# Kernel tuning notes

Measured on AMD Instinct MI355X. Metric: run time of the kernel, lower is better.

## Reference

```python
import jax, jax.numpy as jnp
import numpy as np

B, C, N = 4, 64, 64      # batch, channels (=2*hidden), set size
E = 128                  # set_emb
H = 32                   # hidden_channels


def _unif(k, shape, fan_in):
    lim = 1.0 / np.sqrt(fan_in)
    return jax.random.uniform(k, shape, jnp.float32, -lim, lim)


def setup_inputs() -> dict:
    key = jax.random.key(0)
    ks = jax.random.split(key, 17)
    inp = {"x": jax.random.normal(ks[0], (B, C, N, N), jnp.float32)}
    # set_convs: Linear(4,E) -> ReLU -> Linear(E,E) -> ReLU -> Linear(E,E) -> ReLU -> Linear(E,2)
    inp["W1"] = _unif(ks[1], (4, E), 4);   inp["b1"] = _unif(ks[2], (E,), 4)
    inp["W2"] = _unif(ks[3], (E, E), E);   inp["b2"] = _unif(ks[4], (E,), E)
    inp["W3"] = _unif(ks[5], (E, E), E);   inp["b3"] = _unif(ks[6], (E,), E)
    inp["W4"] = _unif(ks[7], (E, 2), E);   inp["b4"] = _unif(ks[8], (2,), E)
    # channel_fc: 1x1 convs C->128->256->256->H with ReLU between
    inp["Wc1"] = _unif(ks[9], (C, 128), C);     inp["bc1"] = _unif(ks[10], (128,), C)
    inp["Wc2"] = _unif(ks[11], (128, 256), 128); inp["bc2"] = _unif(ks[12], (256,), 128)
    inp["Wc3"] = _unif(ks[13], (256, 256), 256); inp["bc3"] = _unif(ks[14], (256,), 256)
    inp["Wc4"] = _unif(ks[15], (256, H), 256);   inp["bc4"] = _unif(ks[16], (H,), 256)
    return inp


def reference(x, W1, b1, W2, b2, W3, b3, W4, b4,
              Wc1, bc1, Wc2, bc2, Wc3, bc3, Wc4, bc4):
    Bx, Cx, n, _ = x.shape
    # ---- g_x_2to2: gather per-pair 2x2 blocks ----
    d = jnp.diagonal(x, axis1=-2, axis2=-1)              # (B,C,n)
    i = jnp.arange(1, n)[:, None]                        # (n-1,1)
    k = jnp.broadcast_to(jnp.arange(n)[None, :], (n - 1, n))
    j = (k + i) % n                                      # (n-1,n)
    d1 = jnp.broadcast_to(d[:, :, None, :], (Bx, Cx, n - 1, n))  # x[k,k]
    d2 = x[:, :, k, j]                                   # x[k,(k+i)%n]
    d3 = x[:, :, j, k]                                   # x[(k+i)%n,k]
    d4 = d[:, :, j]                                      # x[(k+i)%n,(k+i)%n]
    h = jnp.stack([d1, d2, d3, d4], -1).reshape(Bx, Cx, n * (n - 1), 4)
    # ---- set_convs MLP ----
    h = jax.nn.relu(h @ W1 + b1)
    h = jax.nn.relu(h @ W2 + b2)
    h = jax.nn.relu(h @ W3 + b3)
    h = h @ W4 + b4                                      # (B,C,n(n-1),2)
    # ---- sum_ginv_x_2to2 scatter + coeff ----
    rows = k.reshape(-1)
    cols = j.reshape(-1)
    out = jnp.zeros((Bx, Cx, n, n), x.dtype).at[:, :, rows, cols].set(h[..., 1])
    diag_vals = h[..., 0].reshape(Bx, Cx, n - 1, n).sum(2) / (n - 1)  # coeff diag 1/(n-1)
    out = out + diag_vals[..., :, None] * jnp.eye(n, dtype=x.dtype)
    # ---- channel_fc: 1x1 convs ----
    y = jax.nn.relu(jnp.einsum('bcnm,cd->bdnm', out, Wc1) + bc1[:, None, None])
    y = jax.nn.relu(jnp.einsum('bcnm,cd->bdnm', y, Wc2) + bc2[:, None, None])
    y = jax.nn.relu(jnp.einsum('bcnm,cd->bdnm', y, Wc3) + bc3[:, None, None])
    y = jnp.einsum('bcnm,cd->bdnm', y, Wc4) + bc4[:, None, None]
    return y
```

## Files before the change

kernel.cpp:

```cpp
#include <hip/hip_runtime.h>

typedef __attribute__((ext_vector_type(4))) float f32x4;
typedef __attribute__((ext_vector_type(8))) short s16x8;
typedef __attribute__((ext_vector_type(4))) short s16x4;

__device__ __forceinline__ short f2bf(float f) {
    unsigned u = __builtin_bit_cast(unsigned, f);
    u += 0x7fffu + ((u >> 16) & 1u);
    return (short)(u >> 16);
}
__device__ __forceinline__ short f2bf_fast(float f) {
    unsigned u = __builtin_bit_cast(unsigned, f);
    return (short)((u + 0x8000u) >> 16);
}

__global__ void k_prep(const float* __restrict__ W2, const float* __restrict__ W3,
                       const float* __restrict__ W4,
                       const float* __restrict__ Wc1, const float* __restrict__ Wc2,
                       const float* __restrict__ Wc3, const float* __restrict__ Wc4,
                       short* __restrict__ W2T, short* __restrict__ W3T,
                       float* __restrict__ W4T,
                       short* __restrict__ Wc1T, short* __restrict__ Wc2T,
                       short* __restrict__ Wc3T, short* __restrict__ Wc4T)
{
    int tid = blockIdx.x * 256 + threadIdx.x;
    if (tid < 16384) {
        int n = tid >> 7, k = tid & 127;
        W2T[tid] = f2bf(W2[k * 128 + n]);
        W3T[tid] = f2bf(W3[k * 128 + n]);
    }
    if (tid < 256) {
        int s = tid >> 7, k = tid & 127;
        W4T[tid] = W4[k * 2 + s];
    }
    if (tid < 8192) {
        int n = tid >> 6, c = tid & 63;
        Wc1T[tid] = f2bf(Wc1[c * 128 + n]);
    }
    if (tid < 32768) {
        int n = tid >> 7, k = tid & 127;
        Wc2T[tid] = f2bf(Wc2[k * 256 + n]);
    }
    if (tid < 65536) {
        int n = tid >> 8, k = tid & 255;
        Wc3T[tid] = f2bf(Wc3[k * 256 + n]);
    }
    if (tid < 8192) {
        int n = tid >> 8, k = tid & 255;
        Wc4T[tid] = f2bf(Wc4[k * 32 + n]);
    }
}

__global__ __launch_bounds__(256, 4)
void k_phase1(const float* __restrict__ x,
              const float* __restrict__ W1, const float* __restrict__ b1,
              const short* __restrict__ W2T, const float* __restrict__ b2,
              const short* __restrict__ W3T, const float* __restrict__ b3,
              const float* __restrict__ W4T, const float* __restrict__ b4,
              short* __restrict__ outb, float* __restrict__ diagpart)
{
    __shared__ short hA[64 * 128];
    __shared__ short hB[64 * 128];
    __shared__ float red[4][4][16][2];
    const int t = threadIdx.x;
    const int lane = t & 63;
    const int w = t >> 6;
    const int lr = lane & 15;
    const int hi = lane >> 4;
    const int b = blockIdx.x;
    const int bc = b / 63;
    const int r  = b - bc * 63;

    {
        const int kk = t & 63;
        const int e0 = __builtin_amdgcn_readfirstlane((t >> 6) * 32);
        const int jj = (kk + r + 1) & 63;
        const float* xb = x + bc * 4096;
        float f0 = xb[kk * 65], f1 = xb[kk * 64 + jj];
        float f2 = xb[jj * 64 + kk], f3 = xb[jj * 65];
#pragma unroll
        for (int eo = 0; eo < 32; eo += 8) {
            s16x8 pk;
#pragma unroll
            for (int q = 0; q < 8; ++q) {
                int e = e0 + eo + q;
                float a = fmaf(f3, W1[384 + e], fmaf(f2, W1[256 + e],
                          fmaf(f1, W1[128 + e], fmaf(f0, W1[e], b1[e]))));
                pk[q] = f2bf_fast(fmaxf(a, 0.f));
            }
            int off = (kk * 256 + (e0 + eo) * 2) ^ ((kk & 7) << 4);
            *(s16x8*)((char*)hA + off) = pk;
        }
    }
    __syncthreads();

    const int n0 = w * 32;

    f32x4 acc[4][2] = {};
#pragma unroll
    for (int ks = 0; ks < 4; ++ks) {
        const int kb = ks * 32 + hi * 8;
        s16x8 aw[2], bh[4];
#pragma unroll
        for (int nf = 0; nf < 2; ++nf)
            aw[nf] = *(const s16x8*)(W2T + (n0 + nf * 16 + lr) * 128 + kb);
#pragma unroll
        for (int mf = 0; mf < 4; ++mf) {
            int off = ((mf * 16 + lr) * 256 + kb * 2) ^ ((lr & 7) << 4);
            bh[mf] = *(const s16x8*)((const char*)hA + off);
        }
#pragma unroll
        for (int mf = 0; mf < 4; ++mf)
#pragma unroll
            for (int nf = 0; nf < 2; ++nf)
                acc[mf][nf] = __builtin_amdgcn_mfma_f32_16x16x32_bf16(aw[nf], bh[mf], acc[mf][nf], 0, 0, 0);
    }
    {
        f32x4 bv[2];
#pragma unroll
        for (int nf = 0; nf < 2; ++nf)
            bv[nf] = *(const f32x4*)(b2 + n0 + nf * 16 + 4 * hi);
#pragma unroll
        for (int mf = 0; mf < 4; ++mf) {
            int m = mf * 16 + lr;
#pragma unroll
            for (int nf = 0; nf < 2; ++nf) {
                s16x4 pk;
#pragma unroll
                for (int q = 0; q < 4; ++q)
                    pk[q] = f2bf_fast(fmaxf(acc[mf][nf][q] + bv[nf][q], 0.f));
                int off = (m * 256 + (n0 + nf * 16 + 4 * hi) * 2) ^ ((m & 7) << 4);
                *(s16x4*)((char*)hB + off) = pk;
            }
        }
    }
    __syncthreads();

    f32x4 acc3[4][2] = {};
#pragma unroll
    for (int ks = 0; ks < 4; ++ks) {
        const int kb = ks * 32 + hi * 8;
        s16x8 aw[2], bh[4];
#pragma unroll
        for (int nf = 0; nf < 2; ++nf)
            aw[nf] = *(const s16x8*)(W3T + (n0 + nf * 16 + lr) * 128 + kb);
#pragma unroll
        for (int mf = 0; mf < 4; ++mf) {
            int off = ((mf * 16 + lr) * 256 + kb * 2) ^ ((lr & 7) << 4);
            bh[mf] = *(const s16x8*)((const char*)hB + off);
        }
#pragma unroll
        for (int mf = 0; mf < 4; ++mf)
#pragma unroll
            for (int nf = 0; nf < 2; ++nf)
                acc3[mf][nf] = __builtin_amdgcn_mfma_f32_16x16x32_bf16(aw[nf], bh[mf], acc3[mf][nf], 0, 0, 0);
    }
    {
        f32x4 bv[2], w40[2], w41[2];
#pragma unroll
        for (int nf = 0; nf < 2; ++nf) {
            bv[nf]  = *(const f32x4*)(b3 + n0 + nf * 16 + 4 * hi);
            w40[nf] = *(const f32x4*)(W4T + n0 + nf * 16 + 4 * hi);
            w41[nf] = *(const f32x4*)(W4T + 128 + n0 + nf * 16 + 4 * hi);
        }
#pragma unroll
        for (int mf = 0; mf < 4; ++mf) {
            float s0 = 0.f, s1 = 0.f;
#pragma unroll
            for (int nf = 0; nf < 2; ++nf)
#pragma unroll
                for (int q = 0; q < 4; ++q) {
                    float h = fmaxf(acc3[mf][nf][q] + bv[nf][q], 0.f);
                    s0 = fmaf(h, w40[nf][q], s0);
                    s1 = fmaf(h, w41[nf][q], s1);
                }
            s0 += __shfl_xor(s0, 16, 64); s0 += __shfl_xor(s0, 32, 64);
            s1 += __shfl_xor(s1, 16, 64); s1 += __shfl_xor(s1, 32, 64);
            if (hi == 0) { red[w][mf][lr][0] = s0; red[w][mf][lr][1] = s1; }
        }
    }
    __syncthreads();
    if (t < 128) {
        int k = t & 63, s = t >> 6;
        int mf = k >> 4, lr2 = k & 15;
        float v = red[0][mf][lr2][s] + red[1][mf][lr2][s]
                + red[2][mf][lr2][s] + red[3][mf][lr2][s] + b4[s];
        if (s) {
            int jj = (k + r + 1) & 63;
            outb[bc * 4096 + k * 64 + jj] = f2bf(v);
        } else {
            diagpart[b * 64 + k] = v;
        }
    }
}

__global__ void k_diag(const float* __restrict__ diagpart, short* __restrict__ outb)
{
    __shared__ float rds[256];
    const int t = threadIdx.x, bcq = blockIdx.x;
    const int kx = t & 63, q = t >> 6;
    const float* p = diagpart + bcq * 4032 + kx;
    int r0 = q * 16, r1 = (r0 + 16 < 63) ? r0 + 16 : 63;
    float s = 0.f;
    for (int rr = r0; rr < r1; ++rr) s += p[rr * 64];
    rds[t] = s;
    __syncthreads();
    if (t < 64) {
        float v = (rds[t] + rds[t + 64] + rds[t + 128] + rds[t + 192]) * (1.0f / 63.0f);
        outb[bcq * 4096 + t * 65] = f2bf(v);
    }
}

template<int K, int NT, int NWN, int N_OUT, bool RELU, int SRC, int DST>
__global__ __launch_bounds__(256, 4)
void k_chan(const void* __restrict__ srcv, const short* __restrict__ WT,
            const float* __restrict__ bias, void* __restrict__ dstv)
{
    constexpr int MF = (NWN == 4) ? 2 : 1;
    constexpr int NF = NT / (16 * NWN);
    constexpr int KS = K / 32;
    __shared__ short A[32 * K];
    const int t = threadIdx.x, lane = t & 63, w = t >> 6;
    const int lr = lane & 15, hi = lane >> 4;
    const int m0 = blockIdx.x * 32;
    const int col0 = blockIdx.y * NT;
    const int wn = w & (NWN - 1);
    const int wm = w >> ((NWN == 4) ? 2 : 1);
    const int n0 = col0 + wn * 16 * NF;

    if (SRC == 0) {
        const short* src = (const short*)srcv;
#pragma unroll
        for (int i = t * 8; i < 32 * K; i += 2048) {
            int row = i / K, kk2 = i - row * K;
            s16x8 v = *(const s16x8*)(src + (size_t)m0 * K + i);
            int off = (row * (K * 2) + kk2 * 2) ^ ((row & 7) << 4);
            *(s16x8*)((char*)A + off) = v;
        }
    } else {
        const short* src = (const short*)srcv;
        int bb = blockIdx.x >> 7;
        int nm0 = (blockIdx.x & 127) * 32;
        int c = t & 63, rq = t >> 6;
        s16x8 v = *(const s16x8*)(src + ((size_t)(bb * 64 + c)) * 4096 + nm0 + rq * 8);
#pragma unroll
        for (int q = 0; q < 8; ++q) {
            int row = rq * 8 + q;
            int off = (row * (K * 2) + c * 2) ^ ((row & 7) << 4);
            *(short*)((char*)A + off) = v[q];
        }
    }
    __syncthreads();

    f32x4 acc[MF][NF] = {};
#pragma unroll
    for (int ks = 0; ks < KS; ++ks) {
        const int kb = ks * 32 + hi * 8;
        s16x8 aw[NF], bh[MF];
#pragma unroll
        for (int nf = 0; nf < NF; ++nf)
            aw[nf] = *(const s16x8*)(WT + (size_t)(n0 + nf * 16 + lr) * K + kb);
#pragma unroll
        for (int mf = 0; mf < MF; ++mf) {
            int row = (wm * MF + mf) * 16 + lr;
            int off = (row * (K * 2) + kb * 2) ^ ((lr & 7) << 4);
            bh[mf] = *(const s16x8*)((const char*)A + off);
        }
#pragma unroll
        for (int mf = 0; mf < MF; ++mf)
#pragma unroll
            for (int nf = 0; nf < NF; ++nf)
                acc[mf][nf] = __builtin_amdgcn_mfma_f32_16x16x32_bf16(aw[nf], bh[mf], acc[mf][nf], 0, 0, 0);
    }

    f32x4 bv[NF];
#pragma unroll
    for (int nf = 0; nf < NF; ++nf)
        bv[nf] = *(const f32x4*)(bias + n0 + nf * 16 + 4 * hi);
#pragma unroll
    for (int mf = 0; mf < MF; ++mf) {
        int mrow = (wm * MF + mf) * 16 + lr;
#pragma unroll
        for (int nf = 0; nf < NF; ++nf) {
            if (DST == 0) {
                s16x4 pk;
#pragma unroll
                for (int q = 0; q < 4; ++q) {
                    float v2 = acc[mf][nf][q] + bv[nf][q];
                    if (RELU) v2 = fmaxf(v2, 0.f);
                    pk[q] = f2bf_fast(v2);
                }
                *(s16x4*)((short*)dstv + (size_t)(m0 + mrow) * N_OUT + n0 + nf * 16 + 4 * hi) = pk;
            } else {
                int bb = blockIdx.x >> 7;
                int nm = (blockIdx.x & 127) * 32 + mrow;
#pragma unroll
                for (int q = 0; q < 4; ++q) {
                    int n = n0 + nf * 16 + 4 * hi + q;
                    ((float*)dstv)[(size_t)(bb * 32 + n) * 4096 + nm] = acc[mf][nf][q] + bv[nf][q];
                }
            }
        }
    }
}

extern "C" void kernel_launch(void* const* d_in, const int* in_sizes, int n_in,
                              void* d_out, int out_size, void* d_ws, size_t ws_size,
                              hipStream_t stream)
{
    const float* x   = (const float*)d_in[0];
    const float* W1  = (const float*)d_in[1];
    const float* b1  = (const float*)d_in[2];
    const float* W2  = (const float*)d_in[3];
    const float* b2  = (const float*)d_in[4];
    const float* W3  = (const float*)d_in[5];
    const float* b3  = (const float*)d_in[6];
    const float* W4  = (const float*)d_in[7];
    const float* b4  = (const float*)d_in[8];
    const float* Wc1 = (const float*)d_in[9];
    const float* bc1 = (const float*)d_in[10];
    const float* Wc2 = (const float*)d_in[11];
    const float* bc2 = (const float*)d_in[12];
    const float* Wc3 = (const float*)d_in[13];
    const float* bc3 = (const float*)d_in[14];
    const float* Wc4 = (const float*)d_in[15];
    const float* bc4 = (const float*)d_in[16];
    float* out = (float*)d_out;

    char* ws = (char*)d_ws;
    short* y3       = (short*)(ws);
    short* outb     = (short*)(ws + (8u  << 20));
    float* diagpart = (float*)(ws + (10u << 20));
    short* y2       = (short*)(ws + (8u  << 20));
    short* y1       = (short*)(ws + (16u << 20));

    size_t off = 20u << 20;
    short* W2T  = (short*)(ws + off); off += 16384 * 2;
    short* W3T  = (short*)(ws + off); off += 16384 * 2;
    short* Wc1T = (short*)(ws + off); off += 8192 * 2;
    short* Wc2T = (short*)(ws + off); off += 32768 * 2;
    short* Wc3T = (short*)(ws + off); off += 65536 * 2;
    short* Wc4T = (short*)(ws + off); off += 8192 * 2;
    float* W4T  = (float*)(ws + off); off += 256 * 4;

    k_prep<<<256, 256, 0, stream>>>(W2, W3, W4, Wc1, Wc2, Wc3, Wc4,
                                    W2T, W3T, W4T, Wc1T, Wc2T, Wc3T, Wc4T);
    k_phase1<<<16128, 256, 0, stream>>>(x, W1, b1, W2T, b2, W3T, b3, W4T, b4,
                                        outb, diagpart);
    k_diag<<<256, 256, 0, stream>>>(diagpart, outb);
    k_chan< 64, 128, 4, 128, true,  1, 0><<<dim3(512, 1), 256, 0, stream>>>(outb, Wc1T, bc1, y1);
    k_chan<128, 128, 4, 256, true,  0, 0><<<dim3(512, 2), 256, 0, stream>>>(y1, Wc2T, bc2, y2);
    k_chan<256, 128, 4, 256, true,  0, 0><<<dim3(512, 2), 256, 0, stream>>>(y2, Wc3T, bc3, y3);
    k_chan<256,  32, 2,  32, false, 0, 1><<<dim3(512, 1), 256, 0, stream>>>(y3, Wc4T, bc4, out);
}
```

Measured before the change: 278.9 us.

## Fuse four channel 1x1-conv layers into one kernel and preload MLP weights

Replaces the four separate channel_fc kernels with a single kernel that keeps each 32-row tile's intermediate activations in two shared-memory ping-pong buffers, so the y1/y2/y3 bf16 intermediates never go to global memory. This also cuts three kernel launches. Separately, phase1 now loads all W2/W3 weight fragments into registers up front, before the first GEMM, instead of inside the k-loops. The cost is more register pressure in phase1, which may lower occupancy. The fused kernel has 512 blocks, each computing all output columns, so there is less parallelism per layer.

New measurement: 253.6 us. -9.1%, faster.

```diff
diff --git a/kernel.cpp b/kernel.cpp
--- a/kernel.cpp
+++ b/kernel.cpp
@@ -71,6 +71,17 @@
     const int bc = b / 63;
     const int r  = b - bc * 63;
 
+    const int n0 = w * 32;
+
+    s16x8 aw2[4][2], aw3[4][2];
+#pragma unroll
+    for (int ks = 0; ks < 4; ++ks)
+#pragma unroll
+        for (int nf = 0; nf < 2; ++nf) {
+            aw2[ks][nf] = *(const s16x8*)(W2T + (n0 + nf * 16 + lr) * 128 + ks * 32 + hi * 8);
+            aw3[ks][nf] = *(const s16x8*)(W3T + (n0 + nf * 16 + lr) * 128 + ks * 32 + hi * 8);
+        }
+
     {
         const int kk = t & 63;
         const int e0 = __builtin_amdgcn_readfirstlane((t >> 6) * 32);
@@ -94,16 +105,11 @@
     }
     __syncthreads();
 
-    const int n0 = w * 32;
-
     f32x4 acc[4][2] = {};
 #pragma unroll
     for (int ks = 0; ks < 4; ++ks) {
         const int kb = ks * 32 + hi * 8;
-        s16x8 aw[2], bh[4];
-#pragma unroll
-        for (int nf = 0; nf < 2; ++nf)
-            aw[nf] = *(const s16x8*)(W2T + (n0 + nf * 16 + lr) * 128 + kb);
+        s16x8 bh[4];
 #pragma unroll
         for (int mf = 0; mf < 4; ++mf) {
             int off = ((mf * 16 + lr) * 256 + kb * 2) ^ ((lr & 7) << 4);
@@ -113,7 +119,7 @@
         for (int mf = 0; mf < 4; ++mf)
 #pragma unroll
             for (int nf = 0; nf < 2; ++nf)
-                acc[mf][nf] = __builtin_amdgcn_mfma_f32_16x16x32_bf16(aw[nf], bh[mf], acc[mf][nf], 0, 0, 0);
+                acc[mf][nf] = __builtin_amdgcn_mfma_f32_16x16x32_bf16(aw2[ks][nf], bh[mf], acc[mf][nf], 0, 0, 0);
     }
     {
         f32x4 bv[2];
@@ -140,10 +146,7 @@
 #pragma unroll
     for (int ks = 0; ks < 4; ++ks) {
         const int kb = ks * 32 + hi * 8;
-        s16x8 aw[2], bh[4];
-#pragma unroll
-        for (int nf = 0; nf < 2; ++nf)
-            aw[nf] = *(const s16x8*)(W3T + (n0 + nf * 16 + lr) * 128 + kb);
+        s16x8 bh[4];
 #pragma unroll
         for (int mf = 0; mf < 4; ++mf) {
             int off = ((mf * 16 + lr) * 256 + kb * 2) ^ ((lr & 7) << 4);
@@ -153,7 +156,7 @@
         for (int mf = 0; mf < 4; ++mf)
 #pragma unroll
             for (int nf = 0; nf < 2; ++nf)
-                acc3[mf][nf] = __builtin_amdgcn_mfma_f32_16x16x32_bf16(aw[nf], bh[mf], acc3[mf][nf], 0, 0, 0);
+                acc3[mf][nf] = __builtin_amdgcn_mfma_f32_16x16x32_bf16(aw3[ks][nf], bh[mf], acc3[mf][nf], 0, 0, 0);
     }
     {
         f32x4 bv[2], w40[2], w41[2];
@@ -211,95 +214,106 @@
     }
 }
 
-template<int K, int NT, int NWN, int N_OUT, bool RELU, int SRC, int DST>
+template<int K, int N, bool RELU>
+__device__ __forceinline__ void chan_layer(const short* src, const short* __restrict__ WT,
+                                           const float* __restrict__ bias, short* dst,
+                                           int w, int lr, int hi)
+{
+    constexpr int NF = N / 64;
+    constexpr int KS = K / 32;
+    const int n0 = w * (16 * NF);
+    f32x4 acc[2][NF] = {};
+#pragma unroll
+    for (int ks = 0; ks < KS; ++ks) {
+        const int kb = ks * 32 + hi * 8;
+        s16x8 aw[NF], bh[2];
+#pragma unroll
+        for (int nf = 0; nf < NF; ++nf)
+            aw[nf] = *(const s16x8*)(WT + (n0 + nf * 16 + lr) * K + kb);
+#pragma unroll
+        for (int mf = 0; mf < 2; ++mf) {
+            int off = ((mf * 16 + lr) * (K * 2) + kb * 2) ^ ((lr & 7) << 4);
+            bh[mf] = *(const s16x8*)((const char*)src + off);
+        }
+#pragma unroll
+        for (int mf = 0; mf < 2; ++mf)
+#pragma unroll
+            for (int nf = 0; nf < NF; ++nf)
+                acc[mf][nf] = __builtin_amdgcn_mfma_f32_16x16x32_bf16(aw[nf], bh[mf], acc[mf][nf], 0, 0, 0);
+    }
+    f32x4 bv[NF];
+#pragma unroll
+    for (int nf = 0; nf < NF; ++nf)
+        bv[nf] = *(const f32x4*)(bias + n0 + nf * 16 + 4 * hi);
+#pragma unroll
+    for (int mf = 0; mf < 2; ++mf) {
+        int m = mf * 16 + lr;
+#pragma unroll
+        for (int nf = 0; nf < NF; ++nf) {
+            s16x4 pk;
+#pragma unroll
+            for (int q = 0; q < 4; ++q) {
+                float v = acc[mf][nf][q] + bv[nf][q];
+                if (RELU) v = fmaxf(v, 0.f);
+                pk[q] = f2bf_fast(v);
+            }
+            int off = (m * (N * 2) + (n0 + nf * 16 + 4 * hi) * 2) ^ ((m & 7) << 4);
+            *(s16x4*)((char*)dst + off) = pk;
+        }
+    }
+}
+
 __global__ __launch_bounds__(256, 4)
-void k_chan(const void* __restrict__ srcv, const short* __restrict__ WT,
-            const float* __restrict__ bias, void* __restrict__ dstv)
-{
-    constexpr int MF = (NWN == 4) ? 2 : 1;
-    constexpr int NF = NT / (16 * NWN);
-    constexpr int KS = K / 32;
-    __shared__ short A[32 * K];
+void k_chanfused(const short* __restrict__ outb,
+                 const short* __restrict__ Wc1T, const float* __restrict__ bc1,
+                 const short* __restrict__ Wc2T, const float* __restrict__ bc2,
+                 const short* __restrict__ Wc3T, const float* __restrict__ bc3,
+                 const short* __restrict__ Wc4T, const float* __restrict__ bc4,
+                 float* __restrict__ out)
+{
+    __shared__ short bufA[32 * 256];
+    __shared__ short bufB[32 * 256];
     const int t = threadIdx.x, lane = t & 63, w = t >> 6;
     const int lr = lane & 15, hi = lane >> 4;
-    const int m0 = blockIdx.x * 32;
-    const int col0 = blockIdx.y * NT;
-    const int wn = w & (NWN - 1);
-    const int wm = w >> ((NWN == 4) ? 2 : 1);
-    const int n0 = col0 + wn * 16 * NF;
-
-    if (SRC == 0) {
-        const short* src = (const short*)srcv;
-#pragma unroll
-        for (int i = t * 8; i < 32 * K; i += 2048) {
-            int row = i / K, kk2 = i - row * K;
-            s16x8 v = *(const s16x8*)(src + (size_t)m0 * K + i);
-            int off = (row * (K * 2) + kk2 * 2) ^ ((row & 7) << 4);
-            *(s16x8*)((char*)A + off) = v;
-        }
-    } else {
-        const short* src = (const short*)srcv;
-        int bb = blockIdx.x >> 7;
-        int nm0 = (blockIdx.x & 127) * 32;
+    const int bb = blockIdx.x >> 7;
+    const int nm0 = (blockIdx.x & 127) * 32;
+
+    {
         int c = t & 63, rq = t >> 6;
-        s16x8 v = *(const s16x8*)(src + ((size_t)(bb * 64 + c)) * 4096 + nm0 + rq * 8);
+        s16x8 v = *(const s16x8*)(outb + ((size_t)(bb * 64 + c)) * 4096 + nm0 + rq * 8);
 #pragma unroll
         for (int q = 0; q < 8; ++q) {
             int row = rq * 8 + q;
-            int off = (row * (K * 2) + c * 2) ^ ((row & 7) << 4);
-            *(short*)((char*)A + off) = v[q];
-        }
-    }
-    __syncthreads();
-
-    f32x4 acc[MF][NF] = {};
-#pragma unroll
-    for (int ks = 0; ks < KS; ++ks) {
-        const int kb = ks * 32 + hi * 8;
-        s16x8 aw[NF], bh[MF];
-#pragma unroll
-        for (int nf = 0; nf < NF; ++nf)
-            aw[nf] = *(const s16x8*)(WT + (size_t)(n0 + nf * 16 + lr) * K + kb);
-#pragma unroll
-        for (int mf = 0; mf < MF; ++mf) {
-            int row = (wm * MF + mf) * 16 + lr;
-            int off = (row * (K * 2) + kb * 2) ^ ((lr & 7) << 4);
-            bh[mf] = *(const s16x8*)((const char*)A + off);
-        }
-#pragma unroll
-        for (int mf = 0; mf < MF; ++mf)
-#pragma unroll
-            for (int nf = 0; nf < NF; ++nf)
-                acc[mf][nf] = __builtin_amdgcn_mfma_f32_16x16x32_bf16(aw[nf], bh[mf], acc[mf][nf], 0, 0, 0);
-    }
-
-    f32x4 bv[NF];
-#pragma unroll
-    for (int nf = 0; nf < NF; ++nf)
-        bv[nf] = *(const f32x4*)(bias + n0 + nf * 16 + 4 * hi);
-#pragma unroll
-    for (int mf = 0; mf < MF; ++mf) {
-        int mrow = (wm * MF + mf) * 16 + lr;
-#pragma unroll
-        for (int nf = 0; nf < NF; ++nf) {
-            if (DST == 0) {
-                s16x4 pk;
-#pragma unroll
-                for (int q = 0; q < 4; ++q) {
-                    float v2 = acc[mf][nf][q] + bv[nf][q];
-                    if (RELU) v2 = fmaxf(v2, 0.f);
-                    pk[q] = f2bf_fast(v2);
-                }
-                *(s16x4*)((short*)dstv + (size_t)(m0 + mrow) * N_OUT + n0 + nf * 16 + 4 * hi) = pk;
-            } else {
-                int bb = blockIdx.x >> 7;
-                int nm = (blockIdx.x & 127) * 32 + mrow;
-#pragma unroll
-                for (int q = 0; q < 4; ++q) {
-                    int n = n0 + nf * 16 + 4 * hi + q;
-                    ((float*)dstv)[(size_t)(bb * 32 + n) * 4096 + nm] = acc[mf][nf][q] + bv[nf][q];
-                }
-            }
+            int off = (row * 128 + c * 2) ^ ((row & 7) << 4);
+            *(short*)((char*)bufA + off) = v[q];
+        }
+    }
+    __syncthreads();
+    chan_layer< 64, 128, true>(bufA, Wc1T, bc1, bufB, w, lr, hi);
+    __syncthreads();
+    chan_layer<128, 256, true>(bufB, Wc2T, bc2, bufA, w, lr, hi);
+    __syncthreads();
+    chan_layer<256, 256, true>(bufA, Wc3T, bc3, bufB, w, lr, hi);
+    __syncthreads();
+
+    {
+        const int wn = w & 1, wm = w >> 1;
+        const int n0 = wn * 16;
+        f32x4 acc = {};
+#pragma unroll
+        for (int ks = 0; ks < 8; ++ks) {
+            const int kb = ks * 32 + hi * 8;
+            s16x8 aw = *(const s16x8*)(Wc4T + (n0 + lr) * 256 + kb);
+            int off = ((wm * 16 + lr) * 512 + kb * 2) ^ ((lr & 7) << 4);
+            s16x8 bh = *(const s16x8*)((const char*)bufB + off);
+            acc = __builtin_amdgcn_mfma_f32_16x16x32_bf16(aw, bh, acc, 0, 0, 0);
+        }
+        f32x4 bv = *(const f32x4*)(bc4 + n0 + 4 * hi);
+        const int m = wm * 16 + lr;
+#pragma unroll
+        for (int q = 0; q < 4; ++q) {
+            int n = n0 + 4 * hi + q;
+            out[((size_t)(bb * 32 + n)) * 4096 + nm0 + m] = acc[q] + bv[q];
         }
     }
 }
@@ -328,13 +342,10 @@
     float* out = (float*)d_out;
 
     char* ws = (char*)d_ws;
-    short* y3       = (short*)(ws);
-    short* outb     = (short*)(ws + (8u  << 20));
-    float* diagpart = (float*)(ws + (10u << 20));
-    short* y2       = (short*)(ws + (8u  << 20));
-    short* y1       = (short*)(ws + (16u << 20));
-
-    size_t off = 20u << 20;
+    short* outb     = (short*)(ws);
+    float* diagpart = (float*)(ws + (2u << 20));
+
+    size_t off = 8u << 20;
     short* W2T  = (short*)(ws + off); off += 16384 * 2;
     short* W3T  = (short*)(ws + off); off += 16384 * 2;
     short* Wc1T = (short*)(ws + off); off += 8192 * 2;
@@ -348,8 +359,6 @@
     k_phase1<<<16128, 256, 0, stream>>>(x, W1, b1, W2T, b2, W3T, b3, W4T, b4,
                                         outb, diagpart);
     k_diag<<<256, 256, 0, stream>>>(diagpart, outb);
-    k_chan< 64, 128, 4, 128, true,  1, 0><<<dim3(512, 1), 256, 0, stream>>>(outb, Wc1T, bc1, y1);
-    k_chan<128, 128, 4, 256, true,  0, 0><<<dim3(512, 2), 256, 0, stream>>>(y1, Wc2T, bc2, y2);
-    k_chan<256, 128, 4, 256, true,  0, 0><<<dim3(512, 2), 256, 0, stream>>>(y2, Wc3T, bc3, y3);
-    k_chan<256,  32, 2,  32, false, 0, 1><<<dim3(512, 1), 256, 0, stream>>>(y3, Wc4T, bc4, out);
-}
+    k_chanfused<<<512, 256, 0, stream>>>(outb, Wc1T, bc1, Wc2T, bc2,
+                                         Wc3T, bc3, Wc4T, bc4, out);
+}
```
